# Performance work log

Measured on AMD Instinct MI355X. Metric: run time of the kernel, lower is better.

Reference implementation:

```python
import jax, jax.numpy as jnp
import numpy as np

DIM = 2048
THRESH = 0.33

def _ternary(w):
    # sign() with dead zone: {-1, 0, +1}; detached from grad (matches torch.no_grad)
    return jax.lax.stop_gradient(jnp.where(jnp.abs(w) < THRESH, 0.0, jnp.sign(w)))

def _bitlinear(x, w, b):
    # F.linear(x, ternary_w, bias): x @ ternary_w.T + b
    return jnp.einsum('bsd,od->bso', x, _ternary(w)) + b

def setup_inputs() -> dict:
    key = jax.random.key(0)
    ks = jax.random.split(key, 6)
    B, S, D = 8, 2048, DIM
    x = jax.random.normal(ks[0], (B, S, D), dtype=jnp.float32)
    h_prev = jax.random.normal(ks[1], (B, S, D), dtype=jnp.float32)
    # BitLinear reset_parameters: uniform(-1, 1); bias zeros
    wf = jax.random.uniform(ks[2], (D, D), minval=-1.0, maxval=1.0, dtype=jnp.float32)
    wc = jax.random.uniform(ks[3], (D, D), minval=-1.0, maxval=1.0, dtype=jnp.float32)
    wg = jax.random.uniform(ks[4], (D, D), minval=-1.0, maxval=1.0, dtype=jnp.float32)
    wo = jax.random.uniform(ks[5], (D, D), minval=-1.0, maxval=1.0, dtype=jnp.float32)
    bf = jnp.zeros((D,), dtype=jnp.float32)
    bc = jnp.zeros((D,), dtype=jnp.float32)
    bg = jnp.zeros((D,), dtype=jnp.float32)
    bo = jnp.zeros((D,), dtype=jnp.float32)
    return {"x": x, "h_prev": h_prev, "wf": wf, "bf": bf, "wc": wc, "bc": bc,
            "wg": wg, "bg": bg, "wo": wo, "bo": bo}

def reference(x, h_prev, wf, bf, wc, bc, wg, bg, wo, bo):
    f = jax.nn.sigmoid(_bitlinear(x, wf, bf))
    c = jax.nn.silu(_bitlinear(x, wc, bc))
    h = f * h_prev + (1.0 - f) * c
    g = jax.nn.sigmoid(_bitlinear(x, wg, bg))
    o = _bitlinear(g * h, wo, bo)
    return (o, h)
```

## Files before the change

### kernel.cpp

```cpp
#include <hip/hip_runtime.h>
#include <hip/hip_bf16.h>
#include <cstdint>

#define DIM   2048
#define MROWS 16384
#define NH    64

typedef __bf16 bf16x8 __attribute__((ext_vector_type(8)));
typedef float  f32x4  __attribute__((ext_vector_type(4)));
typedef unsigned short u16;
typedef unsigned int   u32;

#define BARRIER() asm volatile("s_barrier" ::: "memory")
#define WAITVM(N) asm volatile("s_waitcnt vmcnt(" #N ")" ::: "memory")


__device__ __forceinline__ u16 ternary_bits(float w) {
    u32 u = __float_as_uint(w);
    u16 s = (u16)((u >> 16) & 0x8000u);
    return (__builtin_fabsf(w) < 0.33f) ? (u16)0 : (u16)(0x3F80u | s);
}

__device__ __forceinline__ u16 f2bf_rne(float f) {
    u32 u = __float_as_uint(f);
    u32 r = (u + 0x7FFFu + ((u >> 16) & 1u)) >> 16;
    return (u16)r;
}

__device__ __forceinline__ void gload16(const void* g, void* l) {
    __builtin_amdgcn_global_load_lds(
        (const __attribute__((address_space(1))) void*)g,
        (__attribute__((address_space(3))) void*)l,
        16, 0, 0);
}


__global__ void prep_weights(const float* __restrict__ wf, const float* __restrict__ wc,
                             const float* __restrict__ wg, const float* __restrict__ wo,
                             u16* __restrict__ out) {
    const float* srcs[4] = {wf, wc, wg, wo};
    const float* src = srcs[blockIdx.y];
    u16* dst = out + (size_t)blockIdx.y * (DIM * DIM);
    int e = (blockIdx.x * 256 + threadIdx.x) * 8;
    float4 v0 = *(const float4*)(src + e);
    float4 v1 = *(const float4*)(src + e + 4);
    ushort4 o0, o1;
    o0.x = ternary_bits(v0.x); o0.y = ternary_bits(v0.y);
    o0.z = ternary_bits(v0.z); o0.w = ternary_bits(v0.w);
    o1.x = ternary_bits(v1.x); o1.y = ternary_bits(v1.y);
    o1.z = ternary_bits(v1.z); o1.w = ternary_bits(v1.w);
    *(ushort4*)(dst + e)     = o0;
    *(ushort4*)(dst + e + 4) = o1;
}

__global__ void cast_x(const float* __restrict__ x, u16* __restrict__ xb) {
    size_t e = ((size_t)blockIdx.x * 256 + threadIdx.x) * 8;
    float4 v0 = *(const float4*)(x + e);
    float4 v1 = *(const float4*)(x + e + 4);
    ushort4 o0, o1;
    o0.x = f2bf_rne(v0.x); o0.y = f2bf_rne(v0.y);
    o0.z = f2bf_rne(v0.z); o0.w = f2bf_rne(v0.w);
    o1.x = f2bf_rne(v1.x); o1.y = f2bf_rne(v1.y);
    o1.z = f2bf_rne(v1.z); o1.w = f2bf_rne(v1.w);
    *(ushort4*)(xb + e)     = o0;
    *(ushort4*)(xb + e + 4) = o1;
}


__global__ __launch_bounds__(256, 2) void gemm1(
    const u16* __restrict__ xb,
    const u16* __restrict__ wt,
    const float* __restrict__ bfv_, const float* __restrict__ bcv_, const float* __restrict__ bgv_,
    const float* __restrict__ hprev,
    float* __restrict__ hout,
    u16* __restrict__ gh)
{
    __shared__ __align__(16) u16 lds[2][16384];

    const int tid  = threadIdx.x;
    const int lane = tid & 63;
    const int wave = tid >> 6;
    const int wr   = wave >> 1;
    const int wcq  = wave & 1;

    const int bid  = blockIdx.x;
    const int swz  = (bid & 7) * 256 + (bid >> 3);
    const int brow = (swz & 127) * 128;
    const int bcol = (swz >> 7) * 128;

    const int row64 = tid >> 2;
    const int gc4   = (tid & 3) ^ ((tid >> 3) & 3);
    const int ldst  = tid * 8;

    const int fr  = lane & 15;
    const int hi  = lane >> 4;
    const int csw = (hi ^ ((fr >> 1) & 3)) * 8;

    f32x4 acc[3][4][4] = {};

    const u16* aSrc = xb + (size_t)(brow + row64) * DIM;
    const u16* bSrc = wt + (size_t)(bcol + row64) * DIM;
    const size_t WST = (size_t)DIM * DIM;

    auto issueHalf = [&](int slot, int k0) {
        gload16(aSrc + k0 + gc4 * 8,                        (u16*)&lds[slot][ldst]);
        gload16(aSrc + (size_t)64 * DIM + k0 + gc4 * 8,     (u16*)&lds[slot][2048 + ldst]);
        #pragma unroll
        for (int g = 0; g < 3; ++g) {
            gload16(bSrc + (size_t)g * WST + k0 + gc4 * 8,
                    (u16*)&lds[slot][(2 + 2 * g) * 2048 + ldst]);
            gload16(bSrc + (size_t)g * WST + (size_t)64 * DIM + k0 + gc4 * 8,
                    (u16*)&lds[slot][(3 + 2 * g) * 2048 + ldst]);
        }
    };

    auto rdA = [&](const u16* sl, bf16x8 (&a)[4]) {
        #pragma unroll
        for (int mi = 0; mi < 4; ++mi)
            a[mi] = *(const bf16x8*)(sl + (wr * 64 + mi * 16 + fr) * 32 + csw);
    };

    issueHalf(0, 0);
    WAITVM(0);
    BARRIER();

    #pragma unroll 1
    for (int j = 0; j < NH; ++j) {
        const u16* sl = &lds[j & 1][0];
        bf16x8 a[4];
        rdA(sl, a);
        if (j + 1 < NH) issueHalf((j + 1) & 1, (j + 1) * 32);
        #pragma unroll
        for (int ni = 0; ni < 4; ++ni) {
            bf16x8 b[3];
            #pragma unroll
            for (int g = 0; g < 3; ++g)
                b[g] = *(const bf16x8*)(sl + 4096 + g * 4096 + (wcq * 64 + ni * 16 + fr) * 32 + csw);
            __builtin_amdgcn_s_setprio(1);
            #pragma unroll
            for (int g = 0; g < 3; ++g)
                #pragma unroll
                for (int mi = 0; mi < 4; ++mi)
                    acc[g][mi][ni] = __builtin_amdgcn_mfma_f32_16x16x32_bf16(a[mi], b[g], acc[g][mi][ni], 0, 0, 0);
            __builtin_amdgcn_s_setprio(0);
        }
        if (j + 1 < NH) {
            WAITVM(0);
            BARRIER();
        }
    }

    #pragma unroll
    for (int ni = 0; ni < 4; ++ni) {
        const int col = bcol + wcq * 64 + ni * 16 + fr;
        const float bfv = bfv_[col], bcv = bcv_[col], bgv = bgv_[col];
        #pragma unroll
        for (int mi = 0; mi < 4; ++mi) {
            #pragma unroll
            for (int jj = 0; jj < 4; ++jj) {
                const int row = brow + wr * 64 + mi * 16 + hi * 4 + jj;
                const size_t idx = (size_t)row * DIM + col;
                float pf = acc[0][mi][ni][jj] + bfv;
                float pc = acc[1][mi][ni][jj] + bcv;
                float pg = acc[2][mi][ni][jj] + bgv;
                float f  = 1.f / (1.f + __expf(-pf));
                float cc = pc / (1.f + __expf(-pc));
                float g  = 1.f / (1.f + __expf(-pg));
                float hh = f * hprev[idx] + (1.f - f) * cc;
                hout[idx] = hh;
                gh[idx] = f2bf_rne(g * hh);
            }
        }
    }
}


__global__ __launch_bounds__(512) void gemm2(
    const u16* __restrict__ gh,
    const u16* __restrict__ wot,
    const float* __restrict__ bov_,
    float* __restrict__ oout)
{
    __shared__ __align__(16) u16 lds[3 * 16384];

    const int tid  = threadIdx.x;
    const int lane = tid & 63;
    const int wave = tid >> 6;
    const int wr   = wave >> 2;
    const int wcq  = wave & 3;

    const int bid  = blockIdx.x;
    const int swz  = (bid & 7) * 64 + (bid >> 3);
    const int brow = (swz & 63) * 256;
    const int bcol = (swz >> 6) * 256;

    const int srow = tid >> 2;
    const int gc4  = (tid & 3) ^ ((tid >> 3) & 3);
    const int ldst = tid * 8;

    const int fr  = lane & 15;
    const int hi  = lane >> 4;
    const int csw = (hi ^ ((fr >> 1) & 3)) * 8;

    f32x4 accL[8][2] = {};
    f32x4 accH[8][2] = {};

    const u16* aSrc0 = gh  + (size_t)(brow + srow) * DIM;
    const u16* aSrc1 = gh  + (size_t)(brow + 128 + srow) * DIM;
    const u16* bSrc0 = wot + (size_t)(bcol + srow) * DIM;
    const u16* bSrc1 = wot + (size_t)(bcol + 128 + srow) * DIM;

    auto issueA = [&](int so, int k0) {
        gload16(aSrc0 + k0 + gc4 * 8, (u16*)&lds[so + ldst]);
        gload16(aSrc1 + k0 + gc4 * 8, (u16*)&lds[so + 4096 + ldst]);
    };
    auto issueB = [&](int so, int k0) {
        gload16(bSrc0 + k0 + gc4 * 8, (u16*)&lds[so + 8192 + ldst]);
        gload16(bSrc1 + k0 + gc4 * 8, (u16*)&lds[so + 12288 + ldst]);
    };

    auto rdA = [&](int so, bf16x8 (&a)[8]) {
        #pragma unroll
        for (int mi = 0; mi < 8; ++mi)
            a[mi] = *(const bf16x8*)(&lds[so + (wr * 128 + mi * 16 + fr) * 32 + csw]);
    };
    auto rdBL = [&](int so, bf16x8 (&b)[2]) {
        #pragma unroll
        for (int jn = 0; jn < 2; ++jn)
            b[jn] = *(const bf16x8*)(&lds[so + 8192 + (wcq * 64 + jn * 16 + fr) * 32 + csw]);
    };
    auto rdBH = [&](int so, bf16x8 (&b)[2]) {
        #pragma unroll
        for (int jn = 0; jn < 2; ++jn)
            b[jn] = *(const bf16x8*)(&lds[so + 8192 + (wcq * 64 + (2 + jn) * 16 + fr) * 32 + csw]);
    };
    auto mfma2 = [&](bf16x8 (&a)[8], bf16x8 (&b)[2], f32x4 (&c)[8][2]) {
        __builtin_amdgcn_s_setprio(1);
        #pragma unroll
        for (int jn = 0; jn < 2; ++jn)
            #pragma unroll
            for (int mi = 0; mi < 8; ++mi)
                c[mi][jn] = __builtin_amdgcn_mfma_f32_16x16x32_bf16(a[mi], b[jn], c[mi][jn], 0, 0, 0);
        __builtin_amdgcn_s_setprio(0);
    };

    int so0 = 0, so1 = 16384, so2 = 32768;

    bf16x8 aP[8], bLP[2], aQ[8], bLQ[2], bH[2];

    issueA(so0, 0); issueB(so0, 0);
    issueA(so1, 32); issueB(so1, 32);
    WAITVM(4);
    BARRIER();
    rdA(so0, aP); rdBL(so0, bLP);

    auto step = [&](int h, bf16x8 (&aC)[8], bf16x8 (&bLC)[2],
                    bf16x8 (&aN)[8], bf16x8 (&bLN)[2]) {
        const int kn = (h + 2) * 32;
        rdBH(so0, bH);
        issueA(so2, kn);
        mfma2(aC, bLC, accL);
        WAITVM(2);
        BARRIER();
        rdA(so1, aN); rdBL(so1, bLN);
        issueB(so2, kn);
        mfma2(aC, bH, accH);
        BARRIER();
        int t = so0; so0 = so1; so1 = so2; so2 = t;
    };

    #pragma unroll 1
    for (int h = 0; h < NH - 2; h += 2) {
        step(h,     aP, bLP, aQ, bLQ);
        step(h + 1, aQ, bLQ, aP, bLP);
    }
    {
        rdBH(so0, bH);
        mfma2(aP, bLP, accL);
        WAITVM(0);
        BARRIER();
        rdA(so1, aQ); rdBL(so1, bLQ);
        mfma2(aP, bH, accH);
        BARRIER();
        int t = so0; so0 = so1; so1 = so2; so2 = t;
    }
    {
        rdBH(so0, bH);
        mfma2(aQ, bLQ, accL);
        mfma2(aQ, bH, accH);
    }

    auto epi2 = [&](int nbase, f32x4 (&c)[8][2]) {
        #pragma unroll
        for (int jn = 0; jn < 2; ++jn) {
            const int col = bcol + wcq * 64 + (nbase + jn) * 16 + fr;
            const float bov = bov_[col];
            #pragma unroll
            for (int mi = 0; mi < 8; ++mi)
                #pragma unroll
                for (int j = 0; j < 4; ++j)
                    oout[(size_t)(brow + wr * 128 + mi * 16 + hi * 4 + j) * DIM + col] = c[mi][jn][j] + bov;
        }
    };
    epi2(0, accL);
    epi2(2, accH);
}

extern "C" void kernel_launch(void* const* d_in, const int* in_sizes, int n_in,
                              void* d_out, int out_size, void* d_ws, size_t ws_size,
                              hipStream_t stream) {
    const float* x  = (const float*)d_in[0];
    const float* hp = (const float*)d_in[1];
    const float* wf = (const float*)d_in[2];
    const float* bf = (const float*)d_in[3];
    const float* wc = (const float*)d_in[4];
    const float* bc = (const float*)d_in[5];
    const float* wg = (const float*)d_in[6];
    const float* bg = (const float*)d_in[7];
    const float* wo = (const float*)d_in[8];
    const float* bo = (const float*)d_in[9];

    float* o_out = (float*)d_out;
    float* h_out = o_out + (size_t)MROWS * DIM;

    u16* w_t  = (u16*)d_ws;
    u16* x_bf = (u16*)((char*)d_ws + 33554432);
    u16* gh   = (u16*)((char*)d_ws + 100663296);

    prep_weights<<<dim3(2048, 4), 256, 0, stream>>>(wf, wc, wg, wo, w_t);
    cast_x<<<dim3(16384), 256, 0, stream>>>(x, x_bf);
    gemm1<<<dim3(2048), 256, 0, stream>>>(x_bf, w_t, bf, bc, bg, hp, h_out, gh);
    gemm2<<<dim3(512), 512, 0, stream>>>(gh, w_t + 3 * (size_t)DIM * DIM, bo, o_out);
}
```

Baseline: 701.5 us.

## Split gate GEMM into large-tile pipelined GEMM plus separate elementwise gate kernel

Replaces the fused three-gate GEMM (128x128 tiles, double-buffered, gate math in the epilogue) with a 256x256-tile, 512-thread, triple-buffered GEMM. It treats the three gate weights as one N=6144 matrix and stores bf16 pre-activations. A new vectorised elementwise kernel then applies bias, sigmoid, SiLU and the state update, and writes h and g*h. The aim is higher MFMA utilisation and better operand reuse in the main GEMM. In exchange it adds an extra round trip of three bf16 planes through memory, reusing the output buffer and the gh workspace as scratch. It also rounds pre-activations to bf16 before the nonlinearities, which costs some precision.

```diff
diff --git a/kernel.cpp b/kernel.cpp
--- a/kernel.cpp
+++ b/kernel.cpp
@@ -5,6 +5,7 @@
 #define DIM   2048
 #define MROWS 16384
 #define NH    64
+#define PLANE (MROWS * (size_t)DIM)
 
 typedef __bf16 bf16x8 __attribute__((ext_vector_type(8)));
 typedef float  f32x4  __attribute__((ext_vector_type(4)));
@@ -25,6 +26,11 @@
     u32 u = __float_as_uint(f);
     u32 r = (u + 0x7FFFu + ((u >> 16) & 1u)) >> 16;
     return (u16)r;
+}
+
+__device__ __forceinline__ float bf2f(u16 v) {
+    u32 u = ((u32)v) << 16;
+    return __uint_as_float(u);
 }
 
 __device__ __forceinline__ void gload16(const void* g, void* l) {
@@ -67,110 +73,195 @@
 }
 
 
-__global__ __launch_bounds__(256, 2) void gemm1(
+__global__ __launch_bounds__(512) void gemm1p(
     const u16* __restrict__ xb,
     const u16* __restrict__ wt,
+    u16* __restrict__ pf,
+    u16* __restrict__ pc,
+    u16* __restrict__ pg)
+{
+    __shared__ __align__(16) u16 lds[3 * 16384];
+
+    const int tid  = threadIdx.x;
+    const int lane = tid & 63;
+    const int wave = tid >> 6;
+    const int wr   = wave >> 2;
+    const int wcq  = wave & 3;
+
+    const int bid   = blockIdx.x;
+    const int swz   = (bid & 7) * 192 + (bid >> 3);
+    const int mtile = swz & 63;
+    const int ntile = swz >> 6;
+    const int brow  = mtile * 256;
+    const int bcol  = ntile * 256;
+
+    const int srow = tid >> 2;
+    const int gc4  = (tid & 3) ^ ((tid >> 3) & 3);
+    const int ldst = tid * 8;
+
+    const int fr  = lane & 15;
+    const int hi  = lane >> 4;
+    const int csw = (hi ^ ((fr >> 1) & 3)) * 8;
+
+    f32x4 accL[8][2] = {};
+    f32x4 accH[8][2] = {};
+
+    const u16* aSrc0 = xb + (size_t)(brow + srow) * DIM;
+    const u16* aSrc1 = xb + (size_t)(brow + 128 + srow) * DIM;
+    const u16* bSrc0 = wt + (size_t)(bcol + srow) * DIM;
+    const u16* bSrc1 = wt + (size_t)(bcol + 128 + srow) * DIM;
+
+    auto issueA = [&](int so, int k0) {
+        gload16(aSrc0 + k0 + gc4 * 8, (u16*)&lds[so + ldst]);
+        gload16(aSrc1 + k0 + gc4 * 8, (u16*)&lds[so + 4096 + ldst]);
+    };
+    auto issueB = [&](int so, int k0) {
+        gload16(bSrc0 + k0 + gc4 * 8, (u16*)&lds[so + 8192 + ldst]);
+        gload16(bSrc1 + k0 + gc4 * 8, (u16*)&lds[so + 12288 + ldst]);
+    };
+
+    auto rdA = [&](int so, bf16x8 (&a)[8]) {
+        #pragma unroll
+        for (int mi = 0; mi < 8; ++mi)
+            a[mi] = *(const bf16x8*)(&lds[so + (wr * 128 + mi * 16 + fr) * 32 + csw]);
+    };
+    auto rdBL = [&](int so, bf16x8 (&b)[2]) {
+        #pragma unroll
+        for (int jn = 0; jn < 2; ++jn)
+            b[jn] = *(const bf16x8*)(&lds[so + 8192 + (wcq * 64 + jn * 16 + fr) * 32 + csw]);
+    };
+    auto rdBH = [&](int so, bf16x8 (&b)[2]) {
+        #pragma unroll
+        for (int jn = 0; jn < 2; ++jn)
+            b[jn] = *(const bf16x8*)(&lds[so + 8192 + (wcq * 64 + (2 + jn) * 16 + fr) * 32 + csw]);
+    };
+    auto mfma2 = [&](bf16x8 (&a)[8], bf16x8 (&b)[2], f32x4 (&c)[8][2]) {
+        __builtin_amdgcn_s_setprio(1);
+        #pragma unroll
+        for (int jn = 0; jn < 2; ++jn)
+            #pragma unroll
+            for (int mi = 0; mi < 8; ++mi)
+                c[mi][jn] = __builtin_amdgcn_mfma_f32_16x16x32_bf16(a[mi], b[jn], c[mi][jn], 0, 0, 0);
+        __builtin_amdgcn_s_setprio(0);
+    };
+
+    int so0 = 0, so1 = 16384, so2 = 32768;
+
+    bf16x8 aP[8], bLP[2], aQ[8], bLQ[2], bH[2];
+
+    issueA(so0, 0); issueB(so0, 0);
+    issueA(so1, 32); issueB(so1, 32);
+    WAITVM(4);
+    BARRIER();
+    rdA(so0, aP); rdBL(so0, bLP);
+
+    auto step = [&](int h, bf16x8 (&aC)[8], bf16x8 (&bLC)[2],
+                    bf16x8 (&aN)[8], bf16x8 (&bLN)[2]) {
+        const int kn = (h + 2) * 32;
+        rdBH(so0, bH);
+        issueA(so2, kn);
+        mfma2(aC, bLC, accL);
+        WAITVM(2);
+        BARRIER();
+        rdA(so1, aN); rdBL(so1, bLN);
+        issueB(so2, kn);
+        mfma2(aC, bH, accH);
+        BARRIER();
+        int t = so0; so0 = so1; so1 = so2; so2 = t;
+    };
+
+    #pragma unroll 1
+    for (int h = 0; h < NH - 2; h += 2) {
+        step(h,     aP, bLP, aQ, bLQ);
+        step(h + 1, aQ, bLQ, aP, bLP);
+    }
+    {
+        rdBH(so0, bH);
+        mfma2(aP, bLP, accL);
+        WAITVM(0);
+        BARRIER();
+        rdA(so1, aQ); rdBL(so1, bLQ);
+        mfma2(aP, bH, accH);
+        BARRIER();
+        int t = so0; so0 = so1; so1 = so2; so2 = t;
+    }
+    {
+        rdBH(so0, bH);
+        mfma2(aQ, bLQ, accL);
+        mfma2(aQ, bH, accH);
+    }
+
+    const int gate = bcol >> 11;
+    const int colb = bcol & 2047;
+    u16* outp = (gate == 0) ? pf : (gate == 1) ? pc : pg;
+
+    auto epi2 = [&](int nbase, f32x4 (&c)[8][2]) {
+        #pragma unroll
+        for (int jn = 0; jn < 2; ++jn) {
+            const int col = colb + wcq * 64 + (nbase + jn) * 16 + fr;
+            #pragma unroll
+            for (int mi = 0; mi < 8; ++mi)
+                #pragma unroll
+                for (int j = 0; j < 4; ++j)
+                    outp[(size_t)(brow + wr * 128 + mi * 16 + hi * 4 + j) * DIM + col] =
+                        f2bf_rne(c[mi][jn][j]);
+        }
+    };
+    epi2(0, accL);
+    epi2(2, accH);
+}
+
+
+__global__ __launch_bounds__(256) void fuse_gates(
+    const u16* __restrict__ pf, const u16* __restrict__ pc, const u16* __restrict__ pg,
     const float* __restrict__ bfv_, const float* __restrict__ bcv_, const float* __restrict__ bgv_,
     const float* __restrict__ hprev,
     float* __restrict__ hout,
     u16* __restrict__ gh)
 {
-    __shared__ __align__(16) u16 lds[2][16384];
-
-    const int tid  = threadIdx.x;
-    const int lane = tid & 63;
-    const int wave = tid >> 6;
-    const int wr   = wave >> 1;
-    const int wcq  = wave & 1;
-
-    const int bid  = blockIdx.x;
-    const int swz  = (bid & 7) * 256 + (bid >> 3);
-    const int brow = (swz & 127) * 128;
-    const int bcol = (swz >> 7) * 128;
-
-    const int row64 = tid >> 2;
-    const int gc4   = (tid & 3) ^ ((tid >> 3) & 3);
-    const int ldst  = tid * 8;
-
-    const int fr  = lane & 15;
-    const int hi  = lane >> 4;
-    const int csw = (hi ^ ((fr >> 1) & 3)) * 8;
-
-    f32x4 acc[3][4][4] = {};
-
-    const u16* aSrc = xb + (size_t)(brow + row64) * DIM;
-    const u16* bSrc = wt + (size_t)(bcol + row64) * DIM;
-    const size_t WST = (size_t)DIM * DIM;
-
-    auto issueHalf = [&](int slot, int k0) {
-        gload16(aSrc + k0 + gc4 * 8,                        (u16*)&lds[slot][ldst]);
-        gload16(aSrc + (size_t)64 * DIM + k0 + gc4 * 8,     (u16*)&lds[slot][2048 + ldst]);
-        #pragma unroll
-        for (int g = 0; g < 3; ++g) {
-            gload16(bSrc + (size_t)g * WST + k0 + gc4 * 8,
-                    (u16*)&lds[slot][(2 + 2 * g) * 2048 + ldst]);
-            gload16(bSrc + (size_t)g * WST + (size_t)64 * DIM + k0 + gc4 * 8,
-                    (u16*)&lds[slot][(3 + 2 * g) * 2048 + ldst]);
+    #pragma unroll 1
+    for (int it = 0; it < 4; ++it) {
+        const size_t u = (size_t)blockIdx.x * 256 + threadIdx.x + (size_t)it * 1048576;
+        const size_t e = u * 8;
+        const int col = (int)(e & 2047);
+
+        ushort4 f0 = *(const ushort4*)(pf + e), f1 = *(const ushort4*)(pf + e + 4);
+        ushort4 c0 = *(const ushort4*)(pc + e), c1 = *(const ushort4*)(pc + e + 4);
+        ushort4 g0 = *(const ushort4*)(pg + e), g1 = *(const ushort4*)(pg + e + 4);
+        float4 hp0 = *(const float4*)(hprev + e), hp1 = *(const float4*)(hprev + e + 4);
+        float4 bf0 = *(const float4*)(bfv_ + col), bf1 = *(const float4*)(bfv_ + col + 4);
+        float4 bc0 = *(const float4*)(bcv_ + col), bc1 = *(const float4*)(bcv_ + col + 4);
+        float4 bg0 = *(const float4*)(bgv_ + col), bg1 = *(const float4*)(bgv_ + col + 4);
+
+        float4 h0, h1;
+        ushort4 o0, o1;
+
+        #define DO_ELEM(V, HP, PF, PC, PG, BF, BC, BG, OUT)                   \
+        {                                                                      \
+            float pfv = bf2f(PF) + (BF);                                       \
+            float pcv = bf2f(PC) + (BC);                                       \
+            float pgv = bf2f(PG) + (BG);                                       \
+            float f  = 1.f / (1.f + __expf(-pfv));                             \
+            float cc = pcv / (1.f + __expf(-pcv));                             \
+            float g  = 1.f / (1.f + __expf(-pgv));                             \
+            float hh = f * (HP) + (1.f - f) * cc;                              \
+            V = hh;                                                            \
+            OUT = f2bf_rne(g * hh);                                            \
         }
-    };
-
-    auto rdA = [&](const u16* sl, bf16x8 (&a)[4]) {
-        #pragma unroll
-        for (int mi = 0; mi < 4; ++mi)
-            a[mi] = *(const bf16x8*)(sl + (wr * 64 + mi * 16 + fr) * 32 + csw);
-    };
-
-    issueHalf(0, 0);
-    WAITVM(0);
-    BARRIER();
-
-    #pragma unroll 1
-    for (int j = 0; j < NH; ++j) {
-        const u16* sl = &lds[j & 1][0];
-        bf16x8 a[4];
-        rdA(sl, a);
-        if (j + 1 < NH) issueHalf((j + 1) & 1, (j + 1) * 32);
-        #pragma unroll
-        for (int ni = 0; ni < 4; ++ni) {
-            bf16x8 b[3];
-            #pragma unroll
-            for (int g = 0; g < 3; ++g)
-                b[g] = *(const bf16x8*)(sl + 4096 + g * 4096 + (wcq * 64 + ni * 16 + fr) * 32 + csw);
-            __builtin_amdgcn_s_setprio(1);
-            #pragma unroll
-            for (int g = 0; g < 3; ++g)
-                #pragma unroll
-                for (int mi = 0; mi < 4; ++mi)
-                    acc[g][mi][ni] = __builtin_amdgcn_mfma_f32_16x16x32_bf16(a[mi], b[g], acc[g][mi][ni], 0, 0, 0);
-            __builtin_amdgcn_s_setprio(0);
-        }
-        if (j + 1 < NH) {
-            WAITVM(0);
-            BARRIER();
-        }
-    }
-
-    #pragma unroll
-    for (int ni = 0; ni < 4; ++ni) {
-        const int col = bcol + wcq * 64 + ni * 16 + fr;
-        const float bfv = bfv_[col], bcv = bcv_[col], bgv = bgv_[col];
-        #pragma unroll
-        for (int mi = 0; mi < 4; ++mi) {
-            #pragma unroll
-            for (int jj = 0; jj < 4; ++jj) {
-                const int row = brow + wr * 64 + mi * 16 + hi * 4 + jj;
-                const size_t idx = (size_t)row * DIM + col;
-                float pf = acc[0][mi][ni][jj] + bfv;
-                float pc = acc[1][mi][ni][jj] + bcv;
-                float pg = acc[2][mi][ni][jj] + bgv;
-                float f  = 1.f / (1.f + __expf(-pf));
-                float cc = pc / (1.f + __expf(-pc));
-                float g  = 1.f / (1.f + __expf(-pg));
-                float hh = f * hprev[idx] + (1.f - f) * cc;
-                hout[idx] = hh;
-                gh[idx] = f2bf_rne(g * hh);
-            }
-        }
+        DO_ELEM(h0.x, hp0.x, f0.x, c0.x, g0.x, bf0.x, bc0.x, bg0.x, o0.x);
+        DO_ELEM(h0.y, hp0.y, f0.y, c0.y, g0.y, bf0.y, bc0.y, bg0.y, o0.y);
+        DO_ELEM(h0.z, hp0.z, f0.z, c0.z, g0.z, bf0.z, bc0.z, bg0.z, o0.z);
+        DO_ELEM(h0.w, hp0.w, f0.w, c0.w, g0.w, bf0.w, bc0.w, bg0.w, o0.w);
+        DO_ELEM(h1.x, hp1.x, f1.x, c1.x, g1.x, bf1.x, bc1.x, bg1.x, o1.x);
+        DO_ELEM(h1.y, hp1.y, f1.y, c1.y, g1.y, bf1.y, bc1.y, bg1.y, o1.y);
+        DO_ELEM(h1.z, hp1.z, f1.z, c1.z, g1.z, bf1.z, bc1.z, bg1.z, o1.z);
+        DO_ELEM(h1.w, hp1.w, f1.w, c1.w, g1.w, bf1.w, bc1.w, bg1.w, o1.w);
+        #undef DO_ELEM
+
+        *(float4*)(hout + e)     = h0;
+        *(float4*)(hout + e + 4) = h1;
+        *(ushort4*)(gh + e)      = o0;
+        *(ushort4*)(gh + e + 4)  = o1;
     }
 }
 
@@ -321,14 +412,18 @@
     const float* bo = (const float*)d_in[9];
 
     float* o_out = (float*)d_out;
-    float* h_out = o_out + (size_t)MROWS * DIM;
+    float* h_out = o_out + PLANE;
 
     u16* w_t  = (u16*)d_ws;
     u16* x_bf = (u16*)((char*)d_ws + 33554432);
     u16* gh   = (u16*)((char*)d_ws + 100663296);
 
+    u16* p_f = (u16*)o_out;
+    u16* p_c = p_f + PLANE;
+
     prep_weights<<<dim3(2048, 4), 256, 0, stream>>>(wf, wc, wg, wo, w_t);
     cast_x<<<dim3(16384), 256, 0, stream>>>(x, x_bf);
-    gemm1<<<dim3(2048), 256, 0, stream>>>(x_bf, w_t, bf, bc, bg, hp, h_out, gh);
+    gemm1p<<<dim3(1536), 512, 0, stream>>>(x_bf, w_t, p_f, p_c, gh);
+    fuse_gates<<<dim3(4096), 256, 0, stream>>>(p_f, p_c, gh, bf, bc, bg, hp, h_out, gh);
     gemm2<<<dim3(512), 512, 0, stream>>>(gh, w_t + 3 * (size_t)DIM * DIM, bo, o_out);
 }
```

Result: slower. 830.0 us (+18.3%).
